# Kernel optimization log

Measured on AMD Instinct MI355X. Metric: run time of the kernel, lower is better.

The kernel has to match this reference:

```python
import jax, jax.numpy as jnp
import numpy as np
from jax import lax

HIDDEN = 1024; HEADS = 16; HEAD = 64; LAYERS = 4; MLP = 4096
PATCH = 16; TUBE = 2; CROP = 224; FRAMES = 16
GRID = CROP // PATCH          # 14
DEPTH = FRAMES // TUBE        # 8
N_TOK = DEPTH * GRID * GRID   # 1568
EPS = 1e-6
D_ROT = 2 * ((HEAD // 3) // 2)  # 20 per rotary axis (d, h, w); 4 dims left unrotated


def setup_inputs() -> dict:
    key = jax.random.key(0)
    ks = jax.random.split(key, 12)
    w = lambda k, shape: jax.random.normal(k, shape, jnp.float32) * 0.02
    L, H, M = LAYERS, HIDDEN, MLP
    return {
        "pixel_values_videos": jax.random.normal(ks[0], (2, FRAMES, 3, CROP, CROP), jnp.float32),
        "patch_w": w(ks[1], (H, 3, TUBE, PATCH, PATCH)),  # Conv3d OIDHW
        "patch_b": jnp.zeros((H,), jnp.float32),
        "ln1_g": jnp.ones((L, H), jnp.float32), "ln1_b": jnp.zeros((L, H), jnp.float32),
        "qw": w(ks[2], (L, H, H)), "qb": jnp.zeros((L, H), jnp.float32),
        "kw": w(ks[3], (L, H, H)), "kb": jnp.zeros((L, H), jnp.float32),
        "vw": w(ks[4], (L, H, H)), "vb": jnp.zeros((L, H), jnp.float32),
        "pw": w(ks[5], (L, H, H)), "pb": jnp.zeros((L, H), jnp.float32),
        "ln2_g": jnp.ones((L, H), jnp.float32), "ln2_b": jnp.zeros((L, H), jnp.float32),
        "fc1w": w(ks[6], (L, M, H)), "fc1b": jnp.zeros((L, M), jnp.float32),
        "fc2w": w(ks[7], (L, H, M)), "fc2b": jnp.zeros((L, H), jnp.float32),
        "lnf_g": jnp.ones((H,), jnp.float32), "lnf_b": jnp.zeros((H,), jnp.float32),
    }


def _layer_norm(x, g, b):
    mu = jnp.mean(x, axis=-1, keepdims=True)
    var = jnp.mean(jnp.square(x - mu), axis=-1, keepdims=True)
    return (x - mu) * lax.rsqrt(var + EPS) * g + b


def _position_ids():
    ids = jnp.arange(N_TOK)
    tpf = GRID * GRID
    d_pos = ids // tpf
    rem = ids - d_pos * tpf
    h_pos = rem // GRID
    w_pos = rem - h_pos * GRID
    return d_pos, h_pos, w_pos


def _rotate(x, pos):
    # x: (B, H, N, D); matches VJEPA2 rotate_queries_or_keys:
    # tiled (not interleaved) sin/cos * interleaved rotate-half.
    D = x.shape[-1]
    omega = 1.0 / (10000.0 ** (jnp.arange(D // 2, dtype=x.dtype) / (D / 2.0)))
    freq = pos.astype(x.dtype)[:, None] * omega              # (N, D/2)
    sin = jnp.concatenate([jnp.sin(freq)] * 2, axis=-1)      # (N, D) tiled (torch .repeat)
    cos = jnp.concatenate([jnp.cos(freq)] * 2, axis=-1)
    y = x.reshape(x.shape[:-1] + (D // 2, 2))
    y = jnp.stack([-y[..., 1], y[..., 0]], axis=-1).reshape(x.shape)
    return x * cos + y * sin


def _apply_rope(x, pos_ids):
    d_pos, h_pos, w_pos = pos_ids
    s0, s1, s2 = 0, D_ROT, 2 * D_ROT
    parts = [_rotate(x[..., s0:s1], d_pos), _rotate(x[..., s1:s2], h_pos),
             _rotate(x[..., s2:3 * D_ROT], w_pos)]
    if 3 * D_ROT < HEAD:
        parts.append(x[..., 3 * D_ROT:])
    return jnp.concatenate(parts, axis=-1)


def _forward(pixel_values_videos, patch_w, patch_b, ln1_g, ln1_b, qw, qb, kw, kb,
             vw, vb, pw, pb, ln2_g, ln2_b, fc1w, fc1b, fc2w, fc2b, lnf_g, lnf_b):
    B = pixel_values_videos.shape[0]
    x = jnp.transpose(pixel_values_videos, (0, 2, 1, 3, 4))  # (B, C, T, H, W)
    h = lax.conv_general_dilated(x, patch_w, window_strides=(TUBE, PATCH, PATCH),
                                 padding="VALID",
                                 dimension_numbers=("NCDHW", "OIDHW", "NCDHW"))
    h = h + patch_b[None, :, None, None, None]
    h = h.reshape(B, HIDDEN, -1).transpose(0, 2, 1)          # (B, N, HIDDEN)

    pos_ids = _position_ids()
    scale = HEAD ** -0.5

    for i in range(LAYERS):
        # attention block
        xn = _layer_norm(h, ln1_g[i], ln1_b[i])
        def heads(w_, b_):
            return (xn @ w_.T + b_).reshape(B, N_TOK, HEADS, HEAD).transpose(0, 2, 1, 3)
        q = _apply_rope(heads(qw[i], qb[i]), pos_ids)
        k = _apply_rope(heads(kw[i], kb[i]), pos_ids)
        v = heads(vw[i], vb[i])
        aw = jnp.einsum("bhnd,bhmd->bhnm", q, k) * scale
        aw = jax.nn.softmax(aw.astype(jnp.float32), axis=-1).astype(q.dtype)
        o = jnp.einsum("bhnm,bhmd->bhnd", aw, v)
        o = o.transpose(0, 2, 1, 3).reshape(B, N_TOK, HIDDEN)
        h = h + (o @ pw[i].T + pb[i])
        # MLP block
        xn = _layer_norm(h, ln2_g[i], ln2_b[i])
        m = jax.nn.gelu(xn @ fc1w[i].T + fc1b[i], approximate=False)
        h = h + (m @ fc2w[i].T + fc2b[i])

    return _layer_norm(h, lnf_g, lnf_b)


def reference(pixel_values_videos, patch_w, patch_b, ln1_g, ln1_b, qw, qb, kw, kb,
              vw, vb, pw, pb, ln2_g, ln2_b, fc1w, fc1b, fc2w, fc2b, lnf_g, lnf_b):
    return _forward(pixel_values_videos, patch_w, patch_b, ln1_g, ln1_b, qw, qb, kw, kb,
                    vw, vb, pw, pb, ln2_g, ln2_b, fc1w, fc1b, fc2w, fc2b, lnf_g, lnf_b)
```

## Files before the change

kernel.cpp:

```cpp
#include <hip/hip_runtime.h>
#include <math.h>

#define NTOK   1568
#define BATCH  2
#define HID    1024
#define MLPD   4096
#define NLAYER 4
#define ROWS   (BATCH*NTOK)
#define CONVK  1536

typedef __bf16 bf16x8 __attribute__((ext_vector_type(8)));
typedef __bf16 bf16x2 __attribute__((ext_vector_type(2)));
typedef float  f32x4  __attribute__((ext_vector_type(4)));

__device__ __forceinline__ unsigned short f2b(float f) {
  unsigned int u = __float_as_uint(f);
  unsigned int r = u + 0x7FFFu + ((u >> 16) & 1u);
  return (unsigned short)(r >> 16);
}
__device__ __forceinline__ float b2f(unsigned short s) {
  return __uint_as_float((unsigned int)s << 16);
}
__device__ __forceinline__ unsigned cvt2(float a, float b) {
  bf16x2 t;
  t[0] = (__bf16)a;
  t[1] = (__bf16)b;
  return __builtin_bit_cast(unsigned, t);
}
__device__ __forceinline__ float e2(float x) { return __builtin_amdgcn_exp2f(x); }

__device__ __forceinline__ void async16(const unsigned short* g, unsigned short* l) {
  __builtin_amdgcn_global_load_lds(
      (__attribute__((address_space(1))) void*)(void*)g,
      (__attribute__((address_space(3))) void*)(void*)l, 16, 0, 0);
}

__global__ __launch_bounds__(256) void cast4_k(const float* __restrict__ s,
                                               unsigned short* __restrict__ d,
                                               long long n4) {
  long long i = (long long)blockIdx.x * 256 + threadIdx.x;
  long long stride = (long long)gridDim.x * 256;
  for (; i < n4; i += stride) {
    float4 v = ((const float4*)s)[i];
    *(ushort4*)(d + i * 4) = make_ushort4(f2b(v.x), f2b(v.y), f2b(v.z), f2b(v.w));
  }
}

__global__ __launch_bounds__(256) void castqkv_k(const float* __restrict__ q,
                                                 const float* __restrict__ k,
                                                 const float* __restrict__ v,
                                                 unsigned short* __restrict__ dst) {
  const float* src = blockIdx.y == 0 ? q : (blockIdx.y == 1 ? k : v);
  long long i4 = (long long)blockIdx.x * 256 + threadIdx.x;
  long long e = i4 * 4;
  int layer = (int)(e >> 20);
  long long de = e + ((long long)(2 * layer + blockIdx.y) << 20);
  float4 val = ((const float4*)src)[i4];
  *(ushort4*)(dst + de) = make_ushort4(f2b(val.x), f2b(val.y), f2b(val.z), f2b(val.w));
}

__global__ __launch_bounds__(256) void biascat_k(const float* __restrict__ qb,
                                                 const float* __restrict__ kb,
                                                 const float* __restrict__ vb,
                                                 float* __restrict__ dst) {
  int idx = blockIdx.x * 256 + threadIdx.x;
  int layer = idx / 3072, c = idx % 3072;
  float v = c < 1024 ? qb[layer * 1024 + c]
            : (c < 2048 ? kb[layer * 1024 + c - 1024] : vb[layer * 1024 + c - 2048]);
  dst[idx] = v;
}

__global__ __launch_bounds__(256) void im2col_k(const float* __restrict__ pv,
                                                unsigned short* __restrict__ A) {
  int idx = blockIdx.x * 256 + threadIdx.x;
  int row = idx / CONVK, col = idx % CONVK;
  int b = row / NTOK, t = row % NTOK;
  int d = t / 196, r = t % 196, hh = r / 14, ww = r % 14;
  int c = col >> 9, r2 = col & 511, td = r2 >> 8, ph = (r2 >> 4) & 15, pw = r2 & 15;
  int frame = 2 * d + td;
  const float* src = pv + ((((long long)b * 16 + frame) * 3 + c) * 224 + (hh * 16 + ph)) * 224
                        + (ww * 16 + pw);
  A[idx] = f2b(*src);
}

template <int EPI>
__global__ __launch_bounds__(512, 2) void gemm256(const unsigned short* __restrict__ A,
                                                  const unsigned short* __restrict__ B,
                                                  unsigned short* outP,
                                                  int M, int N, int K, int kChunk,
                                                  size_t zStride,
                                                  const float* __restrict__ bias) {
  __shared__ unsigned short As[3][256 * 32];
  __shared__ unsigned short Bs[3][256 * 32];
  const int tid = threadIdx.x;
  const int lane = tid & 63;
  const int w = tid >> 6;
  const int wr = w >> 2, wc = w & 3;
  const int l15 = lane & 15, l4 = lane >> 4;
  const int wbase = tid & ~63;

  const int gx = gridDim.x, gy = gridDim.y;
  const int nwg = gx * gy * (int)gridDim.z;
  int orig = blockIdx.x + gx * (blockIdx.y + gy * blockIdx.z);
  int q = nwg >> 3, r = nwg & 7, xcd = orig & 7, idx = orig >> 3;
  int swz = (xcd < r ? xcd * (q + 1) : r * (q + 1) + (xcd - r) * q) + idx;
  const int bn = swz % gx;
  int tmp = swz / gx;
  const int bm = tmp % gy;
  const int bz = tmp / gy;
  const int kbeg = bz * kChunk;

  const int r0 = tid >> 2;
  const int g0 = (tid & 3) ^ ((tid >> 3) & 3);
  const int i1 = 512 + tid;
  const int r1 = i1 >> 2;
  const int g1 = (tid & 3) ^ ((i1 >> 3) & 3);
  int ra0 = bm * 256 + r0; if (ra0 >= M) ra0 = M - 1;
  int ra1 = bm * 256 + r1; if (ra1 >= M) ra1 = M - 1;
  const int rb0 = bn * 256 + r0;
  const int rb1 = bn * 256 + r1;
  const size_t Ao0 = (size_t)ra0 * K + g0 * 8;
  const size_t Ao1 = (size_t)ra1 * K + g1 * 8;
  const size_t Bo0 = (size_t)rb0 * K + g0 * 8;
  const size_t Bo1 = (size_t)rb1 * K + g1 * 8;

  auto stA = [&](int buf, int k0) {
    async16(A + Ao0 + k0, &As[buf][wbase * 8]);
    async16(A + Ao1 + k0, &As[buf][4096 + wbase * 8]);
  };
  auto stB = [&](int buf, int k0) {
    async16(B + Bo0 + k0, &Bs[buf][wbase * 8]);
    async16(B + Bo1 + k0, &Bs[buf][4096 + wbase * 8]);
  };

  f32x4 acc[8][4] = {};
  const int nk = kChunk >> 5;

  stA(0, kbeg); stB(0, kbeg);
  stA(1, kbeg + 32); stB(1, kbeg + 32);

  const int pchunk = (l4 ^ ((l15 >> 1) & 3)) * 8;
  const int abase = (wr * 128 + l15) * 32 + pchunk;
  const int bbase = (wc * 64 + l15) * 32 + pchunk;

  int cur = 0;
  for (int kt = 0; kt < nk; ++kt) {
    if (kt + 1 < nk) {
      asm volatile("s_waitcnt vmcnt(4)" ::: "memory");
    } else {
      asm volatile("s_waitcnt vmcnt(0)" ::: "memory");
    }
    __builtin_amdgcn_s_barrier();
    __builtin_amdgcn_sched_barrier(0);
    const int prebuf = cur >= 1 ? cur - 1 : 2;
    const bool doPre = (kt + 2 < nk);
    const int kpre = kbeg + (kt + 2) * 32;

    if (doPre) stA(prebuf, kpre);
    bf16x8 bfr[4], af[4];
#pragma unroll
    for (int n = 0; n < 4; ++n)
      bfr[n] = *(const bf16x8*)&Bs[cur][bbase + n * 512];
#pragma unroll
    for (int m = 0; m < 4; ++m)
      af[m] = *(const bf16x8*)&As[cur][abase + m * 512];
    __builtin_amdgcn_s_setprio(1);
#pragma unroll
    for (int m = 0; m < 4; ++m)
#pragma unroll
      for (int n = 0; n < 4; ++n)
        acc[m][n] = __builtin_amdgcn_mfma_f32_16x16x32_bf16(af[m], bfr[n], acc[m][n], 0, 0, 0);
    __builtin_amdgcn_s_setprio(0);
    __builtin_amdgcn_sched_barrier(0);

    if (doPre) stB(prebuf, kpre);
#pragma unroll
    for (int m = 0; m < 4; ++m)
      af[m] = *(const bf16x8*)&As[cur][abase + (m + 4) * 512];
    __builtin_amdgcn_s_setprio(1);
#pragma unroll
    for (int m = 0; m < 4; ++m)
#pragma unroll
      for (int n = 0; n < 4; ++n)
        acc[m + 4][n] = __builtin_amdgcn_mfma_f32_16x16x32_bf16(af[m], bfr[n], acc[m + 4][n], 0, 0, 0);
    __builtin_amdgcn_s_setprio(0);
    __builtin_amdgcn_sched_barrier(0);

    cur = cur == 2 ? 0 : cur + 1;
  }

  float bsv[4] = {0, 0, 0, 0};
  if (EPI >= 1) {
#pragma unroll
    for (int n = 0; n < 4; ++n)
      bsv[n] = bias[bn * 256 + wc * 64 + n * 16 + l15];
  }
  unsigned short* pout = outP + (size_t)bz * zStride;
#pragma unroll
  for (int m = 0; m < 8; ++m) {
    int rowb = bm * 256 + wr * 128 + m * 16 + l4 * 4;
#pragma unroll
    for (int rr2 = 0; rr2 < 4; ++rr2) {
      int rr = rowb + rr2;
      if (rr >= M) continue;
#pragma unroll
      for (int n = 0; n < 4; ++n) {
        int col = bn * 256 + wc * 64 + n * 16 + l15;
        float v = acc[m][n][rr2];
        if (EPI >= 1) v += bsv[n];
        if (EPI == 2) v = 0.5f * v * (1.0f + erff(v * 0.70710678118654752f));
        pout[(size_t)rr * N + col] = f2b(v);
      }
    }
  }
}

template <int NP, int RESID, int FINAL>
__global__ __launch_bounds__(256) void redln_k(const unsigned short* __restrict__ p,
                                               const float* __restrict__ bias,
                                               const float* resid,
                                               const float* __restrict__ g,
                                               const float* __restrict__ b,
                                               float* hOut,
                                               unsigned short* __restrict__ xnOut,
                                               float* __restrict__ fOut,
                                               size_t pStride) {
  __shared__ float red[8];
  const int row = blockIdx.x, tid = threadIdx.x;
  const int col = tid * 4;
  const size_t off = (size_t)row * HID + col;
  float v0 = 0, v1 = 0, v2 = 0, v3 = 0;
#pragma unroll
  for (int pp = 0; pp < NP; ++pp) {
    ushort4 a = *(const ushort4*)(p + (size_t)pp * pStride + off);
    v0 += b2f(a.x); v1 += b2f(a.y); v2 += b2f(a.z); v3 += b2f(a.w);
  }
  float4 bs = *(const float4*)(bias + col);
  v0 += bs.x; v1 += bs.y; v2 += bs.z; v3 += bs.w;
  if (RESID) {
    float4 r = *(const float4*)(resid + off);
    v0 += r.x; v1 += r.y; v2 += r.z; v3 += r.w;
  }
  if (!FINAL) *(float4*)(hOut + off) = make_float4(v0, v1, v2, v3);
  float s = v0 + v1 + v2 + v3;
  float q = v0 * v0 + v1 * v1 + v2 * v2 + v3 * v3;
  for (int o2 = 32; o2; o2 >>= 1) { s += __shfl_xor(s, o2); q += __shfl_xor(q, o2); }
  if ((tid & 63) == 0) { red[tid >> 6] = s; red[4 + (tid >> 6)] = q; }
  __syncthreads();
  float ts = red[0] + red[1] + red[2] + red[3];
  float tq = red[4] + red[5] + red[6] + red[7];
  float mu = ts * (1.0f / HID);
  float var = tq * (1.0f / HID) - mu * mu;
  float rs = rsqrtf(var + 1e-6f);
  float o0 = (v0 - mu) * rs * g[col + 0] + b[col + 0];
  float o1 = (v1 - mu) * rs * g[col + 1] + b[col + 1];
  float o2 = (v2 - mu) * rs * g[col + 2] + b[col + 2];
  float o3 = (v3 - mu) * rs * g[col + 3] + b[col + 3];
  if (FINAL) {
    *(float4*)(fOut + off) = make_float4(o0, o1, o2, o3);
  } else {
    *(ushort4*)(xnOut + off) = make_ushort4(f2b(o0), f2b(o1), f2b(o2), f2b(o3));
  }
}

__global__ __launch_bounds__(256) void qkvprep_k(const unsigned short* __restrict__ qkvb,
                                                 unsigned short* __restrict__ Qh,
                                                 unsigned short* __restrict__ Kh,
                                                 unsigned short* __restrict__ VT) {
  __shared__ unsigned short Vs[64 * 72];
  const int tile = blockIdx.x, bh = blockIdx.y;
  const int b = bh >> 4, head = bh & 15;
  const int tid = threadIdx.x;
  const int tl = tid >> 2, dc = tid & 3;
  const int tg = tile * 64 + tl;
  const int trc = tg < NTOK ? tg : NTOK - 1;
  const bool valid = tg < NTOK;
  const size_t srow = ((size_t)(b * NTOK + trc)) * 3072 + head * 64 + dc * 16;

  {
    uint4 v0 = *(const uint4*)(qkvb + srow + 2048);
    uint4 v1 = *(const uint4*)(qkvb + srow + 2048 + 8);
    *(uint4*)&Vs[tl * 72 + dc * 16] = v0;
    *(uint4*)&Vs[tl * 72 + dc * 16 + 8] = v1;
  }

  const int t = trc;
  const int dpos = t / 196, rem = t - dpos * 196, hpos = rem / 14, wpos = rem - hpos * 14;
  const float LG = 0.9210340371976184f;
  union V16 { uint4 u[2]; unsigned short s[16]; };
  V16 qin, kin, qout, kout;
  qin.u[0] = *(const uint4*)(qkvb + srow);
  qin.u[1] = *(const uint4*)(qkvb + srow + 8);
  kin.u[0] = *(const uint4*)(qkvb + srow + 1024);
  kin.u[1] = *(const uint4*)(qkvb + srow + 1024 + 8);
#pragma unroll
  for (int p = 0; p < 8; ++p) {
    int d0 = dc * 16 + 2 * p;
    float qx0 = b2f(qin.s[2 * p]), qx1 = b2f(qin.s[2 * p + 1]);
    float kx0 = b2f(kin.s[2 * p]), kx1 = b2f(kin.s[2 * p + 1]);
    float qo0, qo1, ko0, ko1;
    if (d0 >= 60) { qo0 = qx0; qo1 = qx1; ko0 = kx0; ko1 = kx1; }
    else {
      int region = d0 / 20;
      int j0 = d0 - region * 20;
      int pos = region == 0 ? dpos : (region == 1 ? hpos : wpos);
      float fp = (float)pos;
      int i0 = j0 % 10, i1 = (j0 + 1) % 10;
      float f0 = expf(-LG * (float)i0) * fp;
      float f1 = expf(-LG * (float)i1) * fp;
      float c0 = cosf(f0), s0 = sinf(f0), c1 = cosf(f1), s1 = sinf(f1);
      qo0 = qx0 * c0 - qx1 * s0; qo1 = qx1 * c1 + qx0 * s1;
      ko0 = kx0 * c0 - kx1 * s0; ko1 = kx1 * c1 + kx0 * s1;
    }
    const float QS = 0.18033688011112042f;
    qout.s[2 * p]     = f2b(qo0 * QS);
    qout.s[2 * p + 1] = f2b(qo1 * QS);
    kout.s[2 * p]     = f2b(ko0);
    kout.s[2 * p + 1] = f2b(ko1);
  }
  if (valid) {
    size_t drow = ((size_t)bh * NTOK + tg) * 64 + dc * 16;
    *(uint4*)(Qh + drow)     = qout.u[0];
    *(uint4*)(Qh + drow + 8) = qout.u[1];
    *(uint4*)(Kh + drow)     = kout.u[0];
    *(uint4*)(Kh + drow + 8) = kout.u[1];
  }
  __syncthreads();
  {
    int d = tid >> 2, tc = tid & 3;
    if (tile * 64 + tc * 16 < NTOK) {
      V16 o;
#pragma unroll
      for (int jj = 0; jj < 16; ++jj) o.s[jj] = Vs[(tc * 16 + jj) * 72 + d];
      unsigned short* dst = VT + ((size_t)bh * 64 + d) * NTOK + tile * 64 + tc * 16;
      *(uint4*)dst = o.u[0];
      *(uint4*)(dst + 8) = o.u[1];
    }
  }
}

#define SM_BLOCK(S, MREG, LREG, OACC, PF)                                        \
  {                                                                              \
    float rmax = S[0][0];                                                        \
    _Pragma("unroll") for (int nt = 0; nt < 4; ++nt)                             \
      _Pragma("unroll") for (int rr = 0; rr < 4; ++rr)                           \
        rmax = fmaxf(rmax, S[nt][rr]);                                           \
    rmax = fmaxf(rmax, __shfl_xor(rmax, 16));                                    \
    rmax = fmaxf(rmax, __shfl_xor(rmax, 32));                                    \
    if (!__all(rmax - MREG <= 11.5f)) {                                          \
      float mn = fmaxf(MREG, rmax);                                              \
      float alpha = e2(MREG - mn);                                               \
      MREG = mn;                                                                 \
      LREG *= alpha;                                                             \
      _Pragma("unroll") for (int dt = 0; dt < 4; ++dt)                           \
        _Pragma("unroll") for (int rr = 0; rr < 4; ++rr) OACC[dt][rr] *= alpha;  \
    }                                                                            \
    float rsum = 0.0f;                                                           \
    _Pragma("unroll") for (int nt = 0; nt < 4; ++nt)                             \
      _Pragma("unroll") for (int rr = 0; rr < 4; ++rr) {                         \
        float pv = e2(S[nt][rr] - MREG);                                         \
        S[nt][rr] = pv;                                                          \
        rsum += pv;                                                              \
      }                                                                          \
    rsum += __shfl_xor(rsum, 16);                                                \
    rsum += __shfl_xor(rsum, 32);                                                \
    LREG += rsum;                                                                \
    unsigned pk01[4], pk23[4];                                                   \
    _Pragma("unroll") for (int nt = 0; nt < 4; ++nt) {                           \
      pk01[nt] = cvt2(S[nt][0], S[nt][1]);                                       \
      pk23[nt] = cvt2(S[nt][2], S[nt][3]);                                       \
    }                                                                            \
    _Pragma("unroll") for (int kc = 0; kc < 2; ++kc) {                           \
      unsigned t0, t1;                                                           \
      t0 = __shfl(pk01[2 * kc], srcA); t1 = __shfl(pk01[2 * kc + 1], srcA);      \
      PF[kc].u[0] = hi ? t1 : t0;                                                \
      t0 = __shfl(pk23[2 * kc], srcA); t1 = __shfl(pk23[2 * kc + 1], srcA);      \
      PF[kc].u[1] = hi ? t1 : t0;                                                \
      t0 = __shfl(pk01[2 * kc], srcB); t1 = __shfl(pk01[2 * kc + 1], srcB);      \
      PF[kc].u[2] = hi ? t1 : t0;                                                \
      t0 = __shfl(pk23[2 * kc], srcB); t1 = __shfl(pk23[2 * kc + 1], srcB);      \
      PF[kc].u[3] = hi ? t1 : t0;                                                \
    }                                                                            \
  }

__global__ __launch_bounds__(256, 3) void flash6_k(const unsigned short* __restrict__ Qh,
                                                   const unsigned short* __restrict__ Kh,
                                                   const unsigned short* __restrict__ VT,
                                                   unsigned short* __restrict__ Opart,
                                                   float2* __restrict__ ml) {
  __shared__ unsigned short Ks[2][64 * 64];
  __shared__ unsigned short Vs[2][64 * 64];
  const int bh = blockIdx.x, qt = blockIdx.y, kv = blockIdx.z;
  const int kt0 = kv ? 13 : 0, kt1 = kv ? 25 : 13;
  const int tid = threadIdx.x, lane = tid & 63, w = tid >> 6;
  const int l15 = lane & 15, l4 = lane >> 4;
  const size_t hb = (size_t)bh * NTOK * 64;
  const unsigned short* kgp = Kh + hb;
  const unsigned short* vbp = VT + (size_t)bh * 64 * NTOK;

  const int srow0 = w * 8 + (lane >> 3);
  const int scg0  = (lane & 7) ^ (srow0 & 7);
  const int srow1 = srow0 + 32;
  const int scg1  = (lane & 7) ^ (srow1 & 7);

  const int qrow0 = qt * 128 + w * 32 + l15;
  const int qrow1 = qrow0 + 16;
  const int qrc0 = qrow0 < NTOK ? qrow0 : NTOK - 1;
  const int qrc1 = qrow1 < NTOK ? qrow1 : NTOK - 1;
  bf16x8 qa0 = *(const bf16x8*)(Qh + hb + (size_t)qrc0 * 64 + l4 * 8);
  bf16x8 qa1 = *(const bf16x8*)(Qh + hb + (size_t)qrc0 * 64 + 32 + l4 * 8);
  bf16x8 qb0 = *(const bf16x8*)(Qh + hb + (size_t)qrc1 * 64 + l4 * 8);
  bf16x8 qb1 = *(const bf16x8*)(Qh + hb + (size_t)qrc1 * 64 + 32 + l4 * 8);

  f32x4 oaccA[4] = {}, oaccB[4] = {};
  float mA = -1e30f, lA = 0.0f, mB = -1e30f, lB = 0.0f;

  {
    const int kc0 = kt0 * 64;
    async16(kgp + (size_t)(kc0 + srow0) * 64 + scg0 * 8, &Ks[0][(size_t)w * 512]);
    async16(kgp + (size_t)(kc0 + srow1) * 64 + scg1 * 8, &Ks[0][(size_t)(w + 4) * 512]);
    async16(vbp + (size_t)srow0 * NTOK + kc0 + scg0 * 8, &Vs[0][(size_t)w * 512]);
    async16(vbp + (size_t)srow1 * NTOK + kc0 + scg1 * 8, &Vs[0][(size_t)(w + 4) * 512]);
  }

  const int h7 = l15 & 7;
  const int p1 = (l4 ^ h7) * 8;
  const int p2 = ((l4 + 4) ^ h7) * 8;
  const int srcA = ((l4 & 1) << 5) | l15;
  const int srcB = srcA + 16;
  const bool hi = (l4 >> 1) != 0;

  for (int kt = kt0; kt < kt1; ++kt) {
    const int cur = (kt - kt0) & 1, nxt = cur ^ 1;
    const int kb = kt * 64;
    __syncthreads();

    if (kt + 1 < kt1) {
      const int kn = kb + 64;
      async16(kgp + (size_t)(kn + srow0) * 64 + scg0 * 8, &Ks[nxt][(size_t)w * 512]);
      async16(kgp + (size_t)(kn + srow1) * 64 + scg1 * 8, &Ks[nxt][(size_t)(w + 4) * 512]);
      async16(vbp + (size_t)srow0 * NTOK + kn + scg0 * 8, &Vs[nxt][(size_t)w * 512]);
      async16(vbp + (size_t)srow1 * NTOK + kn + scg1 * 8, &Vs[nxt][(size_t)(w + 4) * 512]);
    }

    bf16x8 kc0[4], kc1[4];
#pragma unroll
    for (int nt = 0; nt < 4; ++nt) {
      const unsigned short* kr = &Ks[cur][(nt * 16 + l15) * 64];
      kc0[nt] = *(const bf16x8*)(kr + p1);
      kc1[nt] = *(const bf16x8*)(kr + p2);
    }
    f32x4 sA[4] = {}, sB[4] = {};
    __builtin_amdgcn_s_setprio(1);
#pragma unroll
    for (int nt = 0; nt < 4; ++nt) {
      sA[nt] = __builtin_amdgcn_mfma_f32_16x16x32_bf16(kc0[nt], qa0, sA[nt], 0, 0, 0);
      sA[nt] = __builtin_amdgcn_mfma_f32_16x16x32_bf16(kc1[nt], qa1, sA[nt], 0, 0, 0);
      sB[nt] = __builtin_amdgcn_mfma_f32_16x16x32_bf16(kc0[nt], qb0, sB[nt], 0, 0, 0);
      sB[nt] = __builtin_amdgcn_mfma_f32_16x16x32_bf16(kc1[nt], qb1, sB[nt], 0, 0, 0);
    }
    __builtin_amdgcn_s_setprio(0);
    bf16x8 vf0[4], vf1[4];
#pragma unroll
    for (int dt = 0; dt < 4; ++dt) {
      const unsigned short* vr = &Vs[cur][(dt * 16 + l15) * 64];
      vf0[dt] = *(const bf16x8*)(vr + p1);
      vf1[dt] = *(const bf16x8*)(vr + p2);
    }

    if (kb + 64 > NTOK) {
#pragma unroll
      for (int nt = 0; nt < 4; ++nt)
#pragma unroll
        for (int rr = 0; rr < 4; ++rr)
          if (kb + nt * 16 + l4 * 4 + rr >= NTOK) { sA[nt][rr] = -1e30f; sB[nt][rr] = -1e30f; }
    }

    union PB { unsigned u[4]; bf16x8 v; } pfA[2], pfB[2];
    SM_BLOCK(sA, mA, lA, oaccA, pfA)
    __builtin_amdgcn_s_setprio(1);
#pragma unroll
    for (int dt = 0; dt < 4; ++dt) {
      oaccA[dt] = __builtin_amdgcn_mfma_f32_16x16x32_bf16(vf0[dt], pfA[0].v, oaccA[dt], 0, 0, 0);
      oaccA[dt] = __builtin_amdgcn_mfma_f32_16x16x32_bf16(vf1[dt], pfA[1].v, oaccA[dt], 0, 0, 0);
    }
    __builtin_amdgcn_s_setprio(0);
    SM_BLOCK(sB, mB, lB, oaccB, pfB)
    __builtin_amdgcn_s_setprio(1);
#pragma unroll
    for (int dt = 0; dt < 4; ++dt) {
      oaccB[dt] = __builtin_amdgcn_mfma_f32_16x16x32_bf16(vf0[dt], pfB[0].v, oaccB[dt], 0, 0, 0);
      oaccB[dt] = __builtin_amdgcn_mfma_f32_16x16x32_bf16(vf1[dt], pfB[1].v, oaccB[dt], 0, 0, 0);
    }
    __builtin_amdgcn_s_setprio(0);
  }

  __syncthreads();
  unsigned short* Os = &Ks[0][0];
#pragma unroll
  for (int dt = 0; dt < 4; ++dt)
#pragma unroll
    for (int rr = 0; rr < 4; ++rr)
      Os[w * 1152 + l15 * 72 + dt * 16 + l4 * 4 + rr] = f2b(oaccA[dt][rr]);
  if (qrow0 < NTOK) {
    uint4 a  = *(const uint4*)&Os[w * 1152 + l15 * 72 + l4 * 16];
    uint4 bq = *(const uint4*)&Os[w * 1152 + l15 * 72 + l4 * 16 + 8];
    unsigned short* op = Opart + ((size_t)(kv * 32 + bh) * NTOK + qrow0) * 64;
    *(uint4*)(op + l4 * 16) = a;
    *(uint4*)(op + l4 * 16 + 8) = bq;
    if (l4 == 0) ml[(size_t)(kv * 32 + bh) * NTOK + qrow0] = make_float2(mA, lA);
  }
  __builtin_amdgcn_sched_barrier(0);
#pragma unroll
  for (int dt = 0; dt < 4; ++dt)
#pragma unroll
    for (int rr = 0; rr < 4; ++rr)
      Os[w * 1152 + l15 * 72 + dt * 16 + l4 * 4 + rr] = f2b(oaccB[dt][rr]);
  if (qrow1 < NTOK) {
    uint4 a  = *(const uint4*)&Os[w * 1152 + l15 * 72 + l4 * 16];
    uint4 bq = *(const uint4*)&Os[w * 1152 + l15 * 72 + l4 * 16 + 8];
    unsigned short* op = Opart + ((size_t)(kv * 32 + bh) * NTOK + qrow1) * 64;
    *(uint4*)(op + l4 * 16) = a;
    *(uint4*)(op + l4 * 16 + 8) = bq;
    if (l4 == 0) ml[(size_t)(kv * 32 + bh) * NTOK + qrow1] = make_float2(mB, lB);
  }
}

__global__ __launch_bounds__(256) void fcomb_k(const unsigned short* __restrict__ Op,
                                               const float2* __restrict__ ml,
                                               unsigned short* __restrict__ O) {
  const int bh = blockIdx.x, qt = blockIdx.y;
  const int tid = threadIdx.x;
  const int qr = qt * 64 + (tid >> 2);
  const int dc = (tid & 3) * 16;
  if (qr >= NTOK) return;
  const int b = bh >> 4, head = bh & 15;
  float2 a0 = ml[(size_t)bh * NTOK + qr];
  float2 a1 = ml[(size_t)(32 + bh) * NTOK + qr];
  float M = fmaxf(a0.x, a1.x);
  float w0 = e2(a0.x - M), w1 = e2(a1.x - M);
  float inv = 1.0f / (a0.y * w0 + a1.y * w1);
  w0 *= inv; w1 *= inv;
  union V16 { uint4 u[2]; unsigned short s[16]; } p0, p1, o;
  const unsigned short* q0 = Op + ((size_t)bh * NTOK + qr) * 64 + dc;
  const unsigned short* q1 = Op + ((size_t)(32 + bh) * NTOK + qr) * 64 + dc;
  p0.u[0] = *(const uint4*)q0;       p0.u[1] = *(const uint4*)(q0 + 8);
  p1.u[0] = *(const uint4*)q1;       p1.u[1] = *(const uint4*)(q1 + 8);
#pragma unroll
  for (int j = 0; j < 16; ++j) o.s[j] = f2b(b2f(p0.s[j]) * w0 + b2f(p1.s[j]) * w1);
  unsigned short* dst = O + ((size_t)(b * NTOK + qr)) * HID + head * 64 + dc;
  *(uint4*)dst = o.u[0];
  *(uint4*)(dst + 8) = o.u[1];
}

extern "C" void kernel_launch(void* const* d_in, const int* in_sizes, int n_in,
                              void* d_out, int out_size, void* d_ws, size_t ws_size,
                              hipStream_t stream) {
  (void)in_sizes; (void)n_in; (void)out_size; (void)ws_size;
  const float* pv      = (const float*)d_in[0];
  const float* patch_w = (const float*)d_in[1];
  const float* patch_b = (const float*)d_in[2];
  const float* ln1_g   = (const float*)d_in[3];
  const float* ln1_b   = (const float*)d_in[4];
  const float* qw = (const float*)d_in[5];
  const float* qb = (const float*)d_in[6];
  const float* kw = (const float*)d_in[7];
  const float* kb = (const float*)d_in[8];
  const float* vw = (const float*)d_in[9];
  const float* vb = (const float*)d_in[10];
  const float* pw = (const float*)d_in[11];
  const float* pb = (const float*)d_in[12];
  const float* ln2_g = (const float*)d_in[13];
  const float* ln2_b = (const float*)d_in[14];
  const float* fc1w = (const float*)d_in[15];
  const float* fc1b = (const float*)d_in[16];
  const float* fc2w = (const float*)d_in[17];
  const float* fc2b = (const float*)d_in[18];
  const float* lnf_g = (const float*)d_in[19];
  const float* lnf_b = (const float*)d_in[20];

  char* wsp = (char*)d_ws;
  auto alloc = [&](size_t bytes) {
    char* p = wsp;
    wsp += (bytes + 255) & ~(size_t)255;
    return p;
  };
  unsigned short* wPatch = (unsigned short*)alloc((size_t)1024 * 1536 * 2);
  unsigned short* wQKV   = (unsigned short*)alloc((size_t)NLAYER * 3072 * 1024 * 2);
  unsigned short* wP     = (unsigned short*)alloc((size_t)NLAYER * HID * HID * 2);
  unsigned short* wF1    = (unsigned short*)alloc((size_t)NLAYER * MLPD * HID * 2);
  unsigned short* wF2    = (unsigned short*)alloc((size_t)NLAYER * HID * MLPD * 2);
  float*          qkvbias = (float*)alloc((size_t)NLAYER * 3072 * 4);
  unsigned short* Aim  = (unsigned short*)alloc((size_t)ROWS * CONVK * 2);
  float*          h    = (float*)alloc((size_t)ROWS * HID * 4);
  unsigned short* xnb  = (unsigned short*)alloc((size_t)ROWS * HID * 2);
  unsigned short* qkvo = (unsigned short*)alloc((size_t)ROWS * 3072 * 2);
  unsigned short* Qh   = (unsigned short*)alloc((size_t)ROWS * HID * 2 + 8192);
  unsigned short* Kh   = (unsigned short*)alloc((size_t)ROWS * HID * 2 + 8192);
  unsigned short* VT   = (unsigned short*)alloc((size_t)ROWS * HID * 2 + 8192);
  unsigned short* ob   = (unsigned short*)alloc((size_t)ROWS * HID * 2);
  unsigned short* mb   = (unsigned short*)alloc((size_t)ROWS * MLPD * 2);

  unsigned short* part  = Qh;
  unsigned short* partM = mb;
  unsigned short* Opart = mb;
  float2*         mlbuf = (float2*)(mb + (size_t)2 * 32 * NTOK * 64);
  const size_t MNs = (size_t)ROWS * HID;

  auto cast = [&](const float* s, unsigned short* d, long long n) {
    long long n4 = n / 4;
    int grid = (int)((n4 + 255) / 256);
    if (grid > 16384) grid = 16384;
    cast4_k<<<grid, 256, 0, stream>>>(s, d, n4);
  };
  cast(patch_w, wPatch, (long long)1024 * 1536);
  castqkv_k<<<dim3(4096, 3), 256, 0, stream>>>(qw, kw, vw, wQKV);
  cast(pw, wP, (long long)NLAYER * HID * HID);
  cast(fc1w, wF1, (long long)NLAYER * MLPD * HID);
  cast(fc2w, wF2, (long long)NLAYER * HID * MLPD);
  biascat_k<<<48, 256, 0, stream>>>(qb, kb, vb, qkvbias);

  im2col_k<<<(ROWS * CONVK) / 256, 256, 0, stream>>>(pv, Aim);
  gemm256<0><<<dim3(4, 13, 4), 512, 0, stream>>>(
      Aim, wPatch, part, ROWS, HID, CONVK, 384, MNs, nullptr);
  redln_k<4, 0, 0><<<ROWS, 256, 0, stream>>>(
      part, patch_b, nullptr, ln1_g, ln1_b, h, xnb, nullptr, MNs);

  for (int i = 0; i < NLAYER; ++i) {
    gemm256<1><<<dim3(12, 13, 1), 512, 0, stream>>>(
        xnb, wQKV + (size_t)i * 3072 * 1024, qkvo, ROWS, 3072, HID, 1024,
        0, qkvbias + i * 3072);
    qkvprep_k<<<dim3(25, 32), 256, 0, stream>>>(qkvo, Qh, Kh, VT);
    flash6_k<<<dim3(32, 13, 2), 256, 0, stream>>>(Qh, Kh, VT, Opart, mlbuf);
    fcomb_k<<<dim3(32, 25), 256, 0, stream>>>(Opart, mlbuf, ob);
    gemm256<0><<<dim3(4, 13, 4), 512, 0, stream>>>(
        ob, wP + (size_t)i * HID * HID, partM, ROWS, HID, HID, 256, MNs, nullptr);
    redln_k<4, 1, 0><<<ROWS, 256, 0, stream>>>(
        partM, pb + i * HID, h, ln2_g + i * HID, ln2_b + i * HID, h, xnb, nullptr, MNs);
    gemm256<2><<<dim3(16, 13, 1), 512, 0, stream>>>(
        xnb, wF1 + (size_t)i * MLPD * HID, mb, ROWS, MLPD, HID, 1024,
        0, fc1b + i * MLPD);
    gemm256<0><<<dim3(4, 13, 4), 512, 0, stream>>>(
        mb, wF2 + (size_t)i * HID * MLPD, part, ROWS, HID, MLPD, 1024, MNs, nullptr);
    if (i < NLAYER - 1) {
      redln_k<4, 1, 0><<<ROWS, 256, 0, stream>>>(
          part, fc2b + i * HID, h, ln1_g + (i + 1) * HID, ln1_b + (i + 1) * HID,
          h, xnb, nullptr, MNs);
    } else {
      redln_k<4, 1, 1><<<ROWS, 256, 0, stream>>>(
          part, fc2b + i * HID, h, lnf_g, lnf_b, nullptr, nullptr, (float*)d_out, MNs);
    }
  }
}
```

Before: 1.308 ms.

## Deepen async prefetch pipelines in GEMM and flash attention kernels

The GEMM goes from a 3-stage to a 4-stage LDS ring, prefetching three K-tiles ahead with adjusted vmcnt waits, and drops some sched_barriers. The flash attention kernel goes from double to triple buffering of K/V tiles, prefetching two tiles ahead and replacing __syncthreads with an explicit vmcnt wait plus s_barrier. The aim is to hide more global-load latency behind MFMA work. The cost is more LDS per block: 128KB for the GEMM and 48KB for flash. This may limit occupancy, and removing the scheduling barriers can change how the compiler interleaves instructions.

```diff
diff --git a/kernel.cpp b/kernel.cpp
--- a/kernel.cpp
+++ b/kernel.cpp
@@ -90,8 +90,8 @@
                                                   int M, int N, int K, int kChunk,
                                                   size_t zStride,
                                                   const float* __restrict__ bias) {
-  __shared__ unsigned short As[3][256 * 32];
-  __shared__ unsigned short Bs[3][256 * 32];
+  __shared__ unsigned short As[4][256 * 32];
+  __shared__ unsigned short Bs[4][256 * 32];
   const int tid = threadIdx.x;
   const int lane = tid & 63;
   const int w = tid >> 6;
@@ -138,25 +138,28 @@
 
   stA(0, kbeg); stB(0, kbeg);
   stA(1, kbeg + 32); stB(1, kbeg + 32);
+  stA(2, kbeg + 64); stB(2, kbeg + 64);
 
   const int pchunk = (l4 ^ ((l15 >> 1) & 3)) * 8;
   const int abase = (wr * 128 + l15) * 32 + pchunk;
   const int bbase = (wc * 64 + l15) * 32 + pchunk;
 
-  int cur = 0;
   for (int kt = 0; kt < nk; ++kt) {
-    if (kt + 1 < nk) {
+    if (kt < nk - 2) {
+      asm volatile("s_waitcnt vmcnt(8)" ::: "memory");
+    } else if (kt == nk - 2) {
       asm volatile("s_waitcnt vmcnt(4)" ::: "memory");
     } else {
       asm volatile("s_waitcnt vmcnt(0)" ::: "memory");
     }
     __builtin_amdgcn_s_barrier();
     __builtin_amdgcn_sched_barrier(0);
-    const int prebuf = cur >= 1 ? cur - 1 : 2;
-    const bool doPre = (kt + 2 < nk);
-    const int kpre = kbeg + (kt + 2) * 32;
-
-    if (doPre) stA(prebuf, kpre);
+    const int cur = kt & 3;
+    const int pre = (kt + 3) & 3;
+    const bool doPre = (kt + 3 < nk);
+    const int kpre = kbeg + (kt + 3) * 32;
+
+    if (doPre) stA(pre, kpre);
     bf16x8 bfr[4], af[4];
 #pragma unroll
     for (int n = 0; n < 4; ++n)
@@ -171,9 +174,8 @@
       for (int n = 0; n < 4; ++n)
         acc[m][n] = __builtin_amdgcn_mfma_f32_16x16x32_bf16(af[m], bfr[n], acc[m][n], 0, 0, 0);
     __builtin_amdgcn_s_setprio(0);
-    __builtin_amdgcn_sched_barrier(0);
-
-    if (doPre) stB(prebuf, kpre);
+
+    if (doPre) stB(pre, kpre);
 #pragma unroll
     for (int m = 0; m < 4; ++m)
       af[m] = *(const bf16x8*)&As[cur][abase + (m + 4) * 512];
@@ -184,9 +186,6 @@
       for (int n = 0; n < 4; ++n)
         acc[m + 4][n] = __builtin_amdgcn_mfma_f32_16x16x32_bf16(af[m], bfr[n], acc[m + 4][n], 0, 0, 0);
     __builtin_amdgcn_s_setprio(0);
-    __builtin_amdgcn_sched_barrier(0);
-
-    cur = cur == 2 ? 0 : cur + 1;
   }
 
   float bsv[4] = {0, 0, 0, 0};
@@ -388,8 +387,8 @@
                                                    const unsigned short* __restrict__ VT,
                                                    unsigned short* __restrict__ Opart,
                                                    float2* __restrict__ ml) {
-  __shared__ unsigned short Ks[2][64 * 64];
-  __shared__ unsigned short Vs[2][64 * 64];
+  __shared__ unsigned short Ks[3][64 * 64];
+  __shared__ unsigned short Vs[3][64 * 64];
   const int bh = blockIdx.x, qt = blockIdx.y, kv = blockIdx.z;
   const int kt0 = kv ? 13 : 0, kt1 = kv ? 25 : 13;
   const int tid = threadIdx.x, lane = tid & 63, w = tid >> 6;
@@ -402,6 +401,13 @@
   const int scg0  = (lane & 7) ^ (srow0 & 7);
   const int srow1 = srow0 + 32;
   const int scg1  = (lane & 7) ^ (srow1 & 7);
+
+  auto stage = [&](int buf, int kc) {
+    async16(kgp + (size_t)(kc + srow0) * 64 + scg0 * 8, &Ks[buf][(size_t)w * 512]);
+    async16(kgp + (size_t)(kc + srow1) * 64 + scg1 * 8, &Ks[buf][(size_t)(w + 4) * 512]);
+    async16(vbp + (size_t)srow0 * NTOK + kc + scg0 * 8, &Vs[buf][(size_t)w * 512]);
+    async16(vbp + (size_t)srow1 * NTOK + kc + scg1 * 8, &Vs[buf][(size_t)(w + 4) * 512]);
+  };
 
   const int qrow0 = qt * 128 + w * 32 + l15;
   const int qrow1 = qrow0 + 16;
@@ -415,13 +421,8 @@
   f32x4 oaccA[4] = {}, oaccB[4] = {};
   float mA = -1e30f, lA = 0.0f, mB = -1e30f, lB = 0.0f;
 
-  {
-    const int kc0 = kt0 * 64;
-    async16(kgp + (size_t)(kc0 + srow0) * 64 + scg0 * 8, &Ks[0][(size_t)w * 512]);
-    async16(kgp + (size_t)(kc0 + srow1) * 64 + scg1 * 8, &Ks[0][(size_t)(w + 4) * 512]);
-    async16(vbp + (size_t)srow0 * NTOK + kc0 + scg0 * 8, &Vs[0][(size_t)w * 512]);
-    async16(vbp + (size_t)srow1 * NTOK + kc0 + scg1 * 8, &Vs[0][(size_t)(w + 4) * 512]);
-  }
+  stage(0, kt0 * 64);
+  stage(1, (kt0 + 1) * 64);
 
   const int h7 = l15 & 7;
   const int p1 = (l4 ^ h7) * 8;
@@ -430,17 +431,19 @@
   const int srcB = srcA + 16;
   const bool hi = (l4 >> 1) != 0;
 
+  int cur = 0;
   for (int kt = kt0; kt < kt1; ++kt) {
-    const int cur = (kt - kt0) & 1, nxt = cur ^ 1;
     const int kb = kt * 64;
-    __syncthreads();
-
     if (kt + 1 < kt1) {
-      const int kn = kb + 64;
-      async16(kgp + (size_t)(kn + srow0) * 64 + scg0 * 8, &Ks[nxt][(size_t)w * 512]);
-      async16(kgp + (size_t)(kn + srow1) * 64 + scg1 * 8, &Ks[nxt][(size_t)(w + 4) * 512]);
-      async16(vbp + (size_t)srow0 * NTOK + kn + scg0 * 8, &Vs[nxt][(size_t)w * 512]);
-      async16(vbp + (size_t)srow1 * NTOK + kn + scg1 * 8, &Vs[nxt][(size_t)(w + 4) * 512]);
+      asm volatile("s_waitcnt vmcnt(4)" ::: "memory");
+    } else {
+      asm volatile("s_waitcnt vmcnt(0)" ::: "memory");
+    }
+    __builtin_amdgcn_s_barrier();
+    __builtin_amdgcn_sched_barrier(0);
+    if (kt + 2 < kt1) {
+      int nxt2 = cur + 2; if (nxt2 >= 3) nxt2 -= 3;
+      stage(nxt2, (kt + 2) * 64);
     }
 
     bf16x8 kc0[4], kc1[4];
@@ -493,6 +496,7 @@
       oaccB[dt] = __builtin_amdgcn_mfma_f32_16x16x32_bf16(vf1[dt], pfB[1].v, oaccB[dt], 0, 0, 0);
     }
     __builtin_amdgcn_s_setprio(0);
+    cur = cur + 1 == 3 ? 0 : cur + 1;
   }
 
   __syncthreads();
```

Measured after the change: 1.320 ms. No clear change (+0.9%).
